# Kernel optimization log

Measured on AMD Instinct MI355X. Metric: run time of the kernel, lower is better.

Reference implementation:

```python
import jax, jax.numpy as jnp
import numpy as np

SIGMA = 1.0


def setup_inputs() -> dict:
    key = jax.random.key(0)
    z = jax.random.normal(key, (8192, 256), dtype=jnp.float32)
    return {"z": z}


def reference(z):
    n, d = z.shape
    gamma = 1.0 / (2.0 * SIGMA ** 2)
    sq = jnp.sum(z * z, axis=-1)                      # [n]
    gram = z @ z.T                                    # [n, n]
    dist_sq = sq[:, None] + sq[None, :] - 2.0 * gram  # [n, n]
    dist_sq = jnp.maximum(dist_sq, 0.0)
    term_a = jnp.mean(jnp.exp(-gamma * dist_sq))
    denom_b = 1.0 + 2.0 * gamma * SIGMA ** 2
    coeff_b = 1.0 / denom_b ** (d / 2.0)
    term_b = coeff_b * jnp.mean(jnp.exp(-(gamma / denom_b) * sq))
    term_c = 1.0 / (1.0 + 4.0 * gamma * SIGMA ** 2) ** (d / 2.0)
    return term_a - 2.0 * term_b + term_c
```

## Files before the change

### kernel.cpp

```cpp
#include <hip/hip_runtime.h>
#include <math.h>

#define N 8192
#define D 256
#define TILE 128
#define NT (N / TILE)
#define NTILES (NT * (NT + 1) / 2)
#define NPREP (N / 4)
#define LOG2E 1.4426950408889634f
#define GROUP_SZ 4096

#define GLOBAL_AS __attribute__((address_space(1)))
#define LDS_AS    __attribute__((address_space(3)))

typedef float f32x4 __attribute__((ext_vector_type(4)));
typedef int   i32x4 __attribute__((ext_vector_type(4)));
typedef int   i32x8 __attribute__((ext_vector_type(8)));

#define WS_PB_OFF 12288
#define WS_SQ_OFF 32768
#define WS_ZB_OFF 65536

__device__ __forceinline__ size_t frag_off8(int row, int k) {
    const int g = row >> 4, m = row & 15;
    const int ks = (k >> 7) & 1, q = (k >> 5) & 3, j = k & 31;
    return (size_t)g * GROUP_SZ + ks * 2048 + ((j & 16) << 6)
         + (q << 8) + (m << 4) + (j & 15);
}

__global__ __launch_bounds__(256) void prep_kernel(const float* __restrict__ z,
                                                   unsigned char* __restrict__ zb8,
                                                   float* __restrict__ sq,
                                                   float* __restrict__ partialsB) {
    __shared__ float pb4[4];
    const int t = threadIdx.x;
    const int lane = t & 63;
    const int wave = t >> 6;
    const int row = blockIdx.x * 4 + wave;
    float4 v = ((const float4*)(z + (size_t)row * D))[lane];
    unsigned p = __builtin_amdgcn_cvt_pk_fp8_f32(v.x, v.y, 0u, false);
    p = __builtin_amdgcn_cvt_pk_fp8_f32(v.z, v.w, p, true);
    *(unsigned*)(zb8 + frag_off8(row, lane * 4)) = p;
    float s = v.x * v.x + v.y * v.y + v.z * v.z + v.w * v.w;
    #pragma unroll
    for (int off = 32; off > 0; off >>= 1) s += __shfl_xor(s, off, 64);
    if (lane == 0) {
        sq[row] = s;
        pb4[wave] = __expf(-0.25f * s);
    }
    __syncthreads();
    if (t == 0) partialsB[blockIdx.x] = pb4[0] + pb4[1] + pb4[2] + pb4[3];
}

__global__ __launch_bounds__(256) void pair_mfma_kernel(const unsigned char* __restrict__ zb8,
                                                        const float* __restrict__ sq,
                                                        float* __restrict__ partialsA) {
    __shared__ __align__(16) unsigned char As[32768];
    __shared__ __align__(16) unsigned char Bs[32768];

    int bi = 0, rem = blockIdx.x;
    while (rem >= NT - bi) { rem -= NT - bi; ++bi; }
    const int bj = bi + rem;
    const int i0 = bi * TILE, j0 = bj * TILE;

    const int t = threadIdx.x;
    const int lane = t & 63, wave = t >> 6;
    const int wi = wave >> 1, wj = wave & 1;
    const int col = lane & 15, q = lane >> 4;

    const unsigned char* srcA = zb8 + (size_t)(i0 >> 4) * GROUP_SZ;
    const unsigned char* srcB = zb8 + (size_t)(j0 >> 4) * GROUP_SZ;
    #pragma unroll
    for (int i = 0; i < 8; ++i) {
        const int off = (i * 256 + t) * 16;
        __builtin_amdgcn_global_load_lds((const GLOBAL_AS unsigned int*)(srcA + off),
                                         (LDS_AS unsigned int*)(As + off), 16, 0, 0);
        __builtin_amdgcn_global_load_lds((const GLOBAL_AS unsigned int*)(srcB + off),
                                         (LDS_AS unsigned int*)(Bs + off), 16, 0, 0);
    }
    __syncthreads();

    f32x4 acc[4][4];
    #pragma unroll
    for (int mt = 0; mt < 4; ++mt)
        #pragma unroll
        for (int nt = 0; nt < 4; ++nt)
            acc[mt][nt] = (f32x4){0.f, 0.f, 0.f, 0.f};

    #pragma unroll
    for (int ks = 0; ks < 2; ++ks) {
        i32x8 af[4], bf[4];
        #pragma unroll
        for (int x = 0; x < 4; ++x) {
            const unsigned char* a = As + (wi * 4 + x) * GROUP_SZ + ks * 2048 + lane * 16;
            i32x4 lo = *(const i32x4*)a;
            i32x4 hi = *(const i32x4*)(a + 1024);
            af[x] = __builtin_shufflevector(lo, hi, 0, 1, 2, 3, 4, 5, 6, 7);
            const unsigned char* b = Bs + (wj * 4 + x) * GROUP_SZ + ks * 2048 + lane * 16;
            i32x4 blo = *(const i32x4*)b;
            i32x4 bhi = *(const i32x4*)(b + 1024);
            bf[x] = __builtin_shufflevector(blo, bhi, 0, 1, 2, 3, 4, 5, 6, 7);
        }
        #pragma unroll
        for (int mt = 0; mt < 4; ++mt)
            #pragma unroll
            for (int nt = 0; nt < 4; ++nt)
                acc[mt][nt] = __builtin_amdgcn_mfma_scale_f32_16x16x128_f8f6f4(
                    af[mt], bf[nt], acc[mt][nt], 0, 0, 0, 127, 0, 127);
    }

    float cj[4];
    #pragma unroll
    for (int nt = 0; nt < 4; ++nt)
        cj[nt] = -0.5f * LOG2E * sq[j0 + wj * 64 + nt * 16 + col];

    float local = 0.f;
    if (bi != bj) {
        #pragma unroll
        for (int mt = 0; mt < 4; ++mt)
            #pragma unroll
            for (int r = 0; r < 4; ++r) {
                const float ci = -0.5f * LOG2E * sq[i0 + wi * 64 + mt * 16 + q * 4 + r];
                #pragma unroll
                for (int nt = 0; nt < 4; ++nt)
                    local += exp2f(fmaf(acc[mt][nt][r], LOG2E, ci) + cj[nt]);
            }
        local *= 2.f;
    } else {
        #pragma unroll
        for (int mt = 0; mt < 4; ++mt)
            #pragma unroll
            for (int r = 0; r < 4; ++r) {
                const int li = wi * 64 + mt * 16 + q * 4 + r;
                const float ci = -0.5f * LOG2E * sq[i0 + li];
                #pragma unroll
                for (int nt = 0; nt < 4; ++nt) {
                    const int lj = wj * 64 + nt * 16 + col;
                    float arg = fminf(fmaf(acc[mt][nt][r], LOG2E, ci) + cj[nt], 0.f);
                    local += (li == lj) ? 1.0f : exp2f(arg);
                }
            }
    }

    #pragma unroll
    for (int off = 32; off > 0; off >>= 1) local += __shfl_xor(local, off, 64);
    __syncthreads();
    float* red = (float*)As;
    if (lane == 0) red[wave] = local;
    __syncthreads();
    if (t == 0) partialsA[blockIdx.x] = red[0] + red[1] + red[2] + red[3];
}

__global__ __launch_bounds__(256) void final_kernel(const float* __restrict__ partialsA,
                                                    const float* __restrict__ partialsB,
                                                    float* __restrict__ out) {
    __shared__ double redA[4], redB[4];
    const int t = threadIdx.x;
    double sa = 0.0, sb = 0.0;
    for (int i = t; i < NTILES; i += 256) sa += (double)partialsA[i];
    for (int i = t; i < NPREP; i += 256) sb += (double)partialsB[i];
    #pragma unroll
    for (int off = 32; off > 0; off >>= 1) {
        sa += __shfl_xor(sa, off, 64);
        sb += __shfl_xor(sb, off, 64);
    }
    if ((t & 63) == 0) { redA[t >> 6] = sa; redB[t >> 6] = sb; }
    __syncthreads();
    if (t == 0) {
        double A = redA[0] + redA[1] + redA[2] + redA[3];
        double B = redB[0] + redB[1] + redB[2] + redB[3];
        double term_a = A / ((double)N * (double)N);
        double coeff_b = ldexp(1.0, -128);
        double term_c = 1.0;
        for (int i = 0; i < 128; ++i) term_c /= 3.0;
        out[0] = (float)(term_a - 2.0 * coeff_b * (B / (double)N) + term_c);
    }
}

extern "C" void kernel_launch(void* const* d_in, const int* in_sizes, int n_in,
                              void* d_out, int out_size, void* d_ws, size_t ws_size,
                              hipStream_t stream) {
    const float* z = (const float*)d_in[0];
    float* partialsA = (float*)d_ws;
    float* partialsB = (float*)((char*)d_ws + WS_PB_OFF);
    float* sq = (float*)((char*)d_ws + WS_SQ_OFF);
    unsigned char* zb8 = (unsigned char*)((char*)d_ws + WS_ZB_OFF);
    float* out = (float*)d_out;

    hipLaunchKernelGGL(prep_kernel, dim3(NPREP), dim3(256), 0, stream, z, zb8, sq, partialsB);
    hipLaunchKernelGGL(pair_mfma_kernel, dim3(NTILES), dim3(256), 0, stream, zb8, sq, partialsA);
    hipLaunchKernelGGL(final_kernel, dim3(1), dim3(256), 0, stream, partialsA, partialsB, out);
}
```

Before: 90.18 us.

## Fuse prep, pairwise MFMA, and final reduction into one persistent cooperative kernel

Replaces the three-kernel launch with a single cooperative kernel of 256 persistent blocks. The blocks first do the fp8 conversion and squared norms, hit a grid sync, then loop over the triangular tiles, prefetching the next tile's operands into LDS while the second K-half MFMAs and the exp epilogue run. A second grid sync lets block 0 do the final reduction. This is meant to remove launch gaps and overlap loads with compute, at the cost of grid-sync overhead and only 256 blocks, which may leave some CUs idle and make the tile count per block uneven. The old three-kernel path is kept as a fallback if the cooperative launch fails.

```diff
diff --git a/kernel.cpp b/kernel.cpp
--- a/kernel.cpp
+++ b/kernel.cpp
@@ -1,5 +1,8 @@
 #include <hip/hip_runtime.h>
+#include <hip/hip_cooperative_groups.h>
 #include <math.h>
+
+namespace cg = cooperative_groups;
 
 #define N 8192
 #define D 256
@@ -7,6 +10,7 @@
 #define NT (N / TILE)
 #define NTILES (NT * (NT + 1) / 2)
 #define NPREP (N / 4)
+#define NCOOP 256
 #define LOG2E 1.4426950408889634f
 #define GROUP_SZ 4096
 
@@ -17,15 +21,198 @@
 typedef int   i32x4 __attribute__((ext_vector_type(4)));
 typedef int   i32x8 __attribute__((ext_vector_type(8)));
 
-#define WS_PB_OFF 12288
-#define WS_SQ_OFF 32768
-#define WS_ZB_OFF 65536
+#define WS_PAFB_OFF 0
+#define WS_PBFB_OFF 12288
+#define WS_CA_OFF   24576
+#define WS_CB_OFF   28672
+#define WS_SQ_OFF   32768
+#define WS_ZB_OFF   65536
 
 __device__ __forceinline__ size_t frag_off8(int row, int k) {
     const int g = row >> 4, m = row & 15;
     const int ks = (k >> 7) & 1, q = (k >> 5) & 3, j = k & 31;
     return (size_t)g * GROUP_SZ + ks * 2048 + ((j & 16) << 6)
          + (q << 8) + (m << 4) + (j & 15);
+}
+
+__global__ __launch_bounds__(256) void coop_kernel(const float* __restrict__ z,
+                                                   unsigned char* __restrict__ zb8,
+                                                   float* __restrict__ sq,
+                                                   float* __restrict__ coopA,
+                                                   float* __restrict__ coopB,
+                                                   float* __restrict__ out) {
+    __shared__ __align__(16) unsigned char As[32768];
+    __shared__ __align__(16) unsigned char Bs[32768];
+
+    const int t = threadIdx.x;
+    const int lane = t & 63, wave = t >> 6;
+    const int bid = blockIdx.x;
+
+    {
+        float eb = 0.f;
+        #pragma unroll
+        for (int it = 0; it < 8; ++it) {
+            const int row = bid * 32 + wave * 8 + it;
+            float4 v = ((const float4*)(z + (size_t)row * D))[lane];
+            unsigned p = __builtin_amdgcn_cvt_pk_fp8_f32(v.x, v.y, 0u, false);
+            p = __builtin_amdgcn_cvt_pk_fp8_f32(v.z, v.w, p, true);
+            *(unsigned*)(zb8 + frag_off8(row, lane * 4)) = p;
+            float s = v.x * v.x + v.y * v.y + v.z * v.z + v.w * v.w;
+            #pragma unroll
+            for (int off = 32; off > 0; off >>= 1) s += __shfl_xor(s, off, 64);
+            if (lane == 0) { sq[row] = s; eb += __expf(-0.25f * s); }
+        }
+        float* red = (float*)As;
+        if (lane == 0) red[wave] = eb;
+        __syncthreads();
+        if (t == 0) coopB[bid] = red[0] + red[1] + red[2] + red[3];
+    }
+    __threadfence();
+    cg::this_grid().sync();
+
+    const int wi = wave >> 1, wj = wave & 1;
+    const int col = lane & 15, q = lane >> 4;
+    float total = 0.f;
+
+    #define STAGE(TL)  do {                                                        \
+        int sbi = 0, srem = (TL);                                                  \
+        while (srem >= NT - sbi) { srem -= NT - sbi; ++sbi; }                      \
+        const int sbj = sbi + srem;                                                \
+        const unsigned char* sA = zb8 + (size_t)(sbi * 8) * GROUP_SZ;              \
+        const unsigned char* sB = zb8 + (size_t)(sbj * 8) * GROUP_SZ;              \
+        _Pragma("unroll")                                                          \
+        for (int i_ = 0; i_ < 8; ++i_) {                                           \
+            const int off_ = (i_ * 256 + t) * 16;                                  \
+            __builtin_amdgcn_global_load_lds((const GLOBAL_AS unsigned int*)(sA + off_), \
+                                             (LDS_AS unsigned int*)(As + off_), 16, 0, 0); \
+            __builtin_amdgcn_global_load_lds((const GLOBAL_AS unsigned int*)(sB + off_), \
+                                             (LDS_AS unsigned int*)(Bs + off_), 16, 0, 0); \
+        }                                                                          \
+    } while (0)
+
+    STAGE(bid);
+    for (int tile = bid; tile < NTILES; tile += NCOOP) {
+        int bi = 0, rem = tile;
+        while (rem >= NT - bi) { rem -= NT - bi; ++bi; }
+        const int bj = bi + rem;
+        const int i0 = bi * TILE, j0 = bj * TILE;
+
+        f32x4 acc[4][4];
+        #pragma unroll
+        for (int mt = 0; mt < 4; ++mt)
+            #pragma unroll
+            for (int nt = 0; nt < 4; ++nt)
+                acc[mt][nt] = (f32x4){0.f, 0.f, 0.f, 0.f};
+
+        __syncthreads();
+
+        i32x8 af[4], bf[4];
+        #pragma unroll
+        for (int x = 0; x < 4; ++x) {
+            const unsigned char* a = As + (wi * 4 + x) * GROUP_SZ + lane * 16;
+            i32x4 lo = *(const i32x4*)a;
+            i32x4 hi = *(const i32x4*)(a + 1024);
+            af[x] = __builtin_shufflevector(lo, hi, 0, 1, 2, 3, 4, 5, 6, 7);
+            const unsigned char* b = Bs + (wj * 4 + x) * GROUP_SZ + lane * 16;
+            i32x4 blo = *(const i32x4*)b;
+            i32x4 bhi = *(const i32x4*)(b + 1024);
+            bf[x] = __builtin_shufflevector(blo, bhi, 0, 1, 2, 3, 4, 5, 6, 7);
+        }
+        #pragma unroll
+        for (int mt = 0; mt < 4; ++mt)
+            #pragma unroll
+            for (int nt = 0; nt < 4; ++nt)
+                acc[mt][nt] = __builtin_amdgcn_mfma_scale_f32_16x16x128_f8f6f4(
+                    af[mt], bf[nt], acc[mt][nt], 0, 0, 0, 127, 0, 127);
+        #pragma unroll
+        for (int x = 0; x < 4; ++x) {
+            const unsigned char* a = As + (wi * 4 + x) * GROUP_SZ + 2048 + lane * 16;
+            i32x4 lo = *(const i32x4*)a;
+            i32x4 hi = *(const i32x4*)(a + 1024);
+            af[x] = __builtin_shufflevector(lo, hi, 0, 1, 2, 3, 4, 5, 6, 7);
+            const unsigned char* b = Bs + (wj * 4 + x) * GROUP_SZ + 2048 + lane * 16;
+            i32x4 blo = *(const i32x4*)b;
+            i32x4 bhi = *(const i32x4*)(b + 1024);
+            bf[x] = __builtin_shufflevector(blo, bhi, 0, 1, 2, 3, 4, 5, 6, 7);
+        }
+        __syncthreads();
+        if (tile + NCOOP < NTILES) STAGE(tile + NCOOP);
+        #pragma unroll
+        for (int mt = 0; mt < 4; ++mt)
+            #pragma unroll
+            for (int nt = 0; nt < 4; ++nt)
+                acc[mt][nt] = __builtin_amdgcn_mfma_scale_f32_16x16x128_f8f6f4(
+                    af[mt], bf[nt], acc[mt][nt], 0, 0, 0, 127, 0, 127);
+
+        float cj[4];
+        #pragma unroll
+        for (int nt = 0; nt < 4; ++nt)
+            cj[nt] = -0.5f * LOG2E * sq[j0 + wj * 64 + nt * 16 + col];
+
+        float local = 0.f;
+        if (bi != bj) {
+            #pragma unroll
+            for (int mt = 0; mt < 4; ++mt)
+                #pragma unroll
+                for (int r = 0; r < 4; ++r) {
+                    const float ci = -0.5f * LOG2E * sq[i0 + wi * 64 + mt * 16 + q * 4 + r];
+                    #pragma unroll
+                    for (int nt = 0; nt < 4; ++nt)
+                        local += exp2f(fmaf(acc[mt][nt][r], LOG2E, ci) + cj[nt]);
+                }
+            local *= 2.f;
+        } else {
+            #pragma unroll
+            for (int mt = 0; mt < 4; ++mt)
+                #pragma unroll
+                for (int r = 0; r < 4; ++r) {
+                    const int li = wi * 64 + mt * 16 + q * 4 + r;
+                    const float ci = -0.5f * LOG2E * sq[i0 + li];
+                    #pragma unroll
+                    for (int nt = 0; nt < 4; ++nt) {
+                        const int lj = wj * 64 + nt * 16 + col;
+                        float arg = fminf(fmaf(acc[mt][nt][r], LOG2E, ci) + cj[nt], 0.f);
+                        local += (li == lj) ? 1.0f : exp2f(arg);
+                    }
+                }
+        }
+        total += local;
+    }
+    #undef STAGE
+
+    #pragma unroll
+    for (int off = 32; off > 0; off >>= 1) total += __shfl_xor(total, off, 64);
+    __syncthreads();
+    {
+        float* red = (float*)As;
+        if (lane == 0) red[wave] = total;
+        __syncthreads();
+        if (t == 0) coopA[bid] = red[0] + red[1] + red[2] + red[3];
+    }
+    __threadfence();
+    cg::this_grid().sync();
+
+    if (bid == 0) {
+        double* dred = (double*)As;
+        double sa = (double)coopA[t];
+        double sb = (double)coopB[t];
+        #pragma unroll
+        for (int off = 32; off > 0; off >>= 1) {
+            sa += __shfl_xor(sa, off, 64);
+            sb += __shfl_xor(sb, off, 64);
+        }
+        if (lane == 0) { dred[wave] = sa; dred[4 + wave] = sb; }
+        __syncthreads();
+        if (t == 0) {
+            double A = dred[0] + dred[1] + dred[2] + dred[3];
+            double B = dred[4] + dred[5] + dred[6] + dred[7];
+            double term_a = A / ((double)N * (double)N);
+            double coeff_b = ldexp(1.0, -128);
+            double term_c = 1.0;
+            for (int i = 0; i < 128; ++i) term_c /= 3.0;
+            out[0] = (float)(term_a - 2.0 * coeff_b * (B / (double)N) + term_c);
+        }
+    }
 }
 
 __global__ __launch_bounds__(256) void prep_kernel(const float* __restrict__ z,
@@ -181,13 +368,21 @@
                               void* d_out, int out_size, void* d_ws, size_t ws_size,
                               hipStream_t stream) {
     const float* z = (const float*)d_in[0];
-    float* partialsA = (float*)d_ws;
-    float* partialsB = (float*)((char*)d_ws + WS_PB_OFF);
+    float* pA_fb = (float*)((char*)d_ws + WS_PAFB_OFF);
+    float* pB_fb = (float*)((char*)d_ws + WS_PBFB_OFF);
+    float* coopA = (float*)((char*)d_ws + WS_CA_OFF);
+    float* coopB = (float*)((char*)d_ws + WS_CB_OFF);
     float* sq = (float*)((char*)d_ws + WS_SQ_OFF);
     unsigned char* zb8 = (unsigned char*)((char*)d_ws + WS_ZB_OFF);
     float* out = (float*)d_out;
 
-    hipLaunchKernelGGL(prep_kernel, dim3(NPREP), dim3(256), 0, stream, z, zb8, sq, partialsB);
-    hipLaunchKernelGGL(pair_mfma_kernel, dim3(NTILES), dim3(256), 0, stream, zb8, sq, partialsA);
-    hipLaunchKernelGGL(final_kernel, dim3(1), dim3(256), 0, stream, partialsA, partialsB, out);
-}
+    void* args[] = {(void*)&z, (void*)&zb8, (void*)&sq,
+                    (void*)&coopA, (void*)&coopB, (void*)&out};
+    hipError_t e = hipLaunchCooperativeKernel((const void*)coop_kernel, dim3(NCOOP),
+                                              dim3(256), args, 0, stream);
+    if (e != hipSuccess) {
+        hipLaunchKernelGGL(prep_kernel, dim3(NPREP), dim3(256), 0, stream, z, zb8, sq, pB_fb);
+        hipLaunchKernelGGL(pair_mfma_kernel, dim3(NTILES), dim3(256), 0, stream, zb8, sq, pA_fb);
+        hipLaunchKernelGGL(final_kernel, dim3(1), dim3(256), 0, stream, pA_fb, pB_fb, out);
+    }
+}
```

New measurement: 189.7 us. 2.1x slower.
